# Kernel tuning notes

Hardware: AMD Instinct MI355X
Metric: run time of the kernel (lower is better)

The kernel has to match this reference:

```python
import jax, jax.numpy as jnp
import numpy as np
from jax import lax

B, C, H, W = 4, 64, 128, 128
G, K, CO = 8, 3, 64
KK = K * K
MC = G * KK  # mask channels = 72


def _conv3x3(x, w, b):
    # standard 3x3 conv, stride 1, padding 1, NCHW
    y = lax.conv_general_dilated(x, w, (1, 1), ((1, 1), (1, 1)),
                                 dimension_numbers=('NCHW', 'OIHW', 'NCHW'))
    return y + b[None, :, None, None]


def _deform_conv2d(x, offset, mask, w, b):
    """Modulated deformable conv (DCNv2), stride=1, padding=1, dilation=1.
    offset: [B, 2*G*KK, H, W] interpreted as [B, G, KK, 2(dy,dx), H, W] (torchvision layout).
    mask:   [B, G*KK, H, W].
    w: [Co, C/G, K, K], b: [Co].
    """
    Bn, Cn, Hn, Wn = x.shape
    Co, Cg, Kh, Kw = w.shape
    Gn = Cn // Cg
    KKn = Kh * Kw
    Ho, Wo = Hn, Wn  # stride 1, pad 1, k 3

    off = offset.reshape(Bn, Gn, KKn, 2, Ho, Wo)
    dy, dx = off[:, :, :, 0], off[:, :, :, 1]
    m = mask.reshape(Bn, Gn, 1, KKn, Ho, Wo)

    kh = (jnp.arange(KKn) // Kw).astype(x.dtype)  # kernel row index
    kw = (jnp.arange(KKn) % Kw).astype(x.dtype)
    hh = jnp.arange(Ho, dtype=x.dtype)
    ww = jnp.arange(Wo, dtype=x.dtype)
    # sampling positions: h - pad + kh*dil + dy  -> [B,G,KK,Ho,Wo]
    py = hh[None, None, None, :, None] - 1.0 + kh[None, None, :, None, None] + dy
    px = ww[None, None, None, None, :] - 1.0 + kw[None, None, :, None, None] + dx

    y0 = jnp.floor(py); x0 = jnp.floor(px)
    ly = py - y0; lx = px - x0
    y0i = y0.astype(jnp.int32); x0i = x0.astype(jnp.int32)
    y1i = y0i + 1; x1i = x0i + 1

    xg = x.reshape(Bn, Gn, Cg, Hn * Wn)

    def corner(yi, xi, wgt):
        valid = ((yi >= 0) & (yi < Hn) & (xi >= 0) & (xi < Wn)).astype(x.dtype)
        idx = (jnp.clip(yi, 0, Hn - 1) * Wn + jnp.clip(xi, 0, Wn - 1))
        idx = idx.reshape(Bn, Gn, 1, KKn * Ho * Wo)
        v = jnp.take_along_axis(xg, idx, axis=3).reshape(Bn, Gn, Cg, KKn, Ho, Wo)
        return v * (wgt * valid)[:, :, None]

    val = (corner(y0i, x0i, (1.0 - ly) * (1.0 - lx))
           + corner(y0i, x1i, (1.0 - ly) * lx)
           + corner(y1i, x0i, ly * (1.0 - lx))
           + corner(y1i, x1i, ly * lx))
    val = val * m  # modulation

    wr = w.reshape(Gn, Co // Gn, Cg, KKn)
    out = jnp.einsum('bgckhw,gock->bgohw', val, wr).reshape(Bn, Co, Ho, Wo)
    return out + b[None, :, None, None]


def setup_inputs() -> dict:
    key = jax.random.key(0)
    ks = jax.random.split(key, 8)
    f = lambda k, s, sc=1.0: jax.random.normal(k, s, dtype=jnp.float32) * sc
    return {
        'x': f(ks[0], (B, C, H, W)),
        'share_with_feat': f(ks[1], (B, C, H, W)),
        'offset_feat': f(ks[2], (B, C, H, W)),
        # conv_offset_mask: C -> 3*G*KK (zero-init in original; small random here)
        'w_om': f(ks[3], (3 * MC, C, 3, 3), 0.02),
        'b_om': jnp.zeros((3 * MC,), jnp.float32),
        'w_em1': f(ks[4], (C, 2 * C, 3, 3), 0.05),
        'b_em1': jnp.zeros((C,), jnp.float32),
        'w_em2': f(ks[5], (MC, C, 3, 3), 0.05),
        'b_em2': jnp.zeros((MC,), jnp.float32),
        # deform conv weight: [Co, C/G, 3, 3]
        'w_dc': f(ks[6], (CO, C // G, 3, 3), 0.05),
        'b_dc': f(ks[7], (CO,), 0.05),
    }


def reference(x, share_with_feat, offset_feat, w_om, b_om, w_em1, b_em1,
              w_em2, b_em2, w_dc, b_dc):
    om = _conv3x3(offset_feat, w_om, b_om)
    o1, o2, mask_x = jnp.split(om, 3, axis=1)
    offset = jnp.concatenate([o1, o2], axis=1)
    mask_x = jax.nn.sigmoid(mask_x)
    x_deform = _deform_conv2d(x, offset, mask_x, w_dc, b_dc)
    # extra_mask=True branch
    em = _conv3x3(jnp.concatenate([share_with_feat, offset_feat], axis=1), w_em1, b_em1)
    em = jnp.where(em >= 0, em, 0.1 * em)  # LeakyReLU(0.1)
    em = jax.nn.sigmoid(_conv3x3(em, w_em2, b_em2))
    share_deform = _deform_conv2d(share_with_feat, offset, em, w_dc, b_dc)
    return (x_deform, share_deform)
```

## Files before the change

### kernel.cpp

```cpp
#include <hip/hip_runtime.h>
#include <math.h>

#define BB 4
#define CC 64
#define HH 128
#define WW 128
#define GG 8
#define COO 64
#define HWC (HH*WW)

#define DPAD 12
#define DROW 26

typedef float f32x16 __attribute__((ext_vector_type(16)));
typedef __bf16 bf16x8 __attribute__((ext_vector_type(8)));

__device__ __forceinline__ unsigned short bf16_rn(float f) {
    unsigned int u = __float_as_uint(f);
    unsigned int r = (u + 0x7fffu + ((u >> 16) & 1u)) >> 16;
    return (unsigned short)r;
}
__device__ __forceinline__ float b2f(unsigned short u) {
    return __uint_as_float(((unsigned int)u) << 16);
}

__global__ __launch_bounds__(256) void to_c16_kernel(const float* __restrict__ in,
                                                     unsigned short* __restrict__ out) {
    __shared__ unsigned short lds[64][66];
    const int b = blockIdx.y;
    const int pix0 = blockIdx.x * 64;
    const int t = threadIdx.x;
    {
        const int p = t & 63, q = t >> 6;
#pragma unroll
        for (int i = 0; i < 16; i++) {
            int c = i * 4 + q;
            lds[c][p] = bf16_rn(in[((size_t)b * 64 + c) * HWC + pix0 + p]);
        }
    }
    __syncthreads();
    {
        const int pl = t & 63, cg = t >> 6;
        unsigned int u[8];
#pragma unroll
        for (int j = 0; j < 8; j++) {
            unsigned int lo = lds[cg * 16 + 2 * j][pl];
            unsigned int hi = lds[cg * 16 + 2 * j + 1][pl];
            u[j] = lo | (hi << 16);
        }
        unsigned int* dst = (unsigned int*)(out + ((size_t)(b * 4 + cg) * HWC + pix0 + pl) * 16);
        *(uint4*)dst = make_uint4(u[0], u[1], u[2], u[3]);
        *(uint4*)(dst + 4) = make_uint4(u[4], u[5], u[6], u[7]);
    }
}

__global__ __launch_bounds__(256) void pack_xs_kernel(const float* __restrict__ x,
                                                      const float* __restrict__ s,
                                                      unsigned int* __restrict__ xs, int n) {
    int i = blockIdx.x * 256 + threadIdx.x;
    if (i < n) {
        xs[i] = (unsigned int)bf16_rn(x[i]) | ((unsigned int)bf16_rn(s[i]) << 16);
    }
}

__global__ void pack_w_kernel(const float* __restrict__ w, unsigned short* __restrict__ wp,
                              int Cout, int COP, int CinTot, int n) {
    int idx = blockIdx.x * 256 + threadIdx.x;
    if (idx >= n) return;
    int i  = idx & 15;
    int co = (idx >> 4) % COP;
    int t  = idx / (16 * COP);
    int cg = t & 3;
    int kk = (t >> 2) % 9;
    int seg = t / 36;
    int cin = seg * 64 + cg * 16 + i;
    float v = (co < Cout) ? w[((size_t)co * CinTot + cin) * 9 + kk] : 0.f;
    wp[idx] = bf16_rn(v);
}

template<int NSEG>
__global__ __launch_bounds__(256) void conv_mfma_kernel(
    const unsigned short* __restrict__ in0,
    const unsigned short* __restrict__ in1,
    const unsigned short* __restrict__ wp,
    const float* __restrict__ bias,
    void* __restrict__ out,
    int Cout, int COP, int out_mode, int act)
{
    const int lane = threadIdx.x & 63;
    const int wid  = threadIdx.x >> 6;
    const int l31  = lane & 31;
    const int half = lane >> 5;
    const int b    = blockIdx.x >> 5;
    const int r    = ((blockIdx.x & 31) << 2) + wid;
    const int co0  = blockIdx.y * 32;

    f32x16 acc[4];
#pragma unroll
    for (int nt = 0; nt < 4; nt++)
#pragma unroll
        for (int rg = 0; rg < 16; rg++) acc[nt][rg] = 0.f;

    bf16x8 bz;
#pragma unroll
    for (int i = 0; i < 8; i++) bz[i] = (__bf16)0.f;

#pragma unroll
    for (int seg = 0; seg < NSEG; seg++) {
        const unsigned short* in = seg ? in1 : in0;
        const unsigned short* inb = in + (size_t)b * 4 * HWC * 16;
        for (int kk = 0; kk < 9; kk++) {
            const int rr = r + kk / 3 - 1;
            if ((unsigned)rr < (unsigned)HH) {
                const int dxo = kk % 3 - 1;
#pragma unroll
                for (int cg = 0; cg < 4; cg++) {
                    bf16x8 afrag = *(const bf16x8*)(wp +
                        ((size_t)(((seg * 9 + kk) * 4 + cg) * COP + co0 + l31) * 16 + half * 8));
                    const size_t plane = ((size_t)cg * HWC + (size_t)rr * WW) * 16;
#pragma unroll
                    for (int nt = 0; nt < 4; nt++) {
                        const int cc = nt * 32 + l31 + dxo;
                        bf16x8 bfrag = bz;
                        if ((unsigned)cc < (unsigned)WW)
                            bfrag = *(const bf16x8*)(inb + plane + (size_t)cc * 16 + half * 8);
                        acc[nt] = __builtin_amdgcn_mfma_f32_32x32x16_bf16(afrag, bfrag, acc[nt], 0, 0, 0);
                    }
                }
            }
        }
    }

#pragma unroll
    for (int nt = 0; nt < 4; nt++) {
#pragma unroll
        for (int rg = 0; rg < 16; rg++) {
            const int row = (rg & 3) + 8 * (rg >> 2) + 4 * half;
            const int co = co0 + row;
            if (co < Cout) {
                float v = acc[nt][rg] + bias[co];
                if (act == 1)      v = (v >= 0.f) ? v : 0.1f * v;
                else if (act == 2) v = 1.f / (1.f + __expf(-v));
                else if (act == 3 && co >= 144) v = 1.f / (1.f + __expf(-v));
                const int pix = r * WW + nt * 32 + l31;
                if (out_mode == 2)
                    ((unsigned short*)out)[((size_t)b * Cout + co) * HWC + pix] = bf16_rn(v);
                else
                    ((unsigned short*)out)[((size_t)(b * 4 + (co >> 4)) * HWC + pix) * 16 + (co & 15)] = bf16_rn(v);
            }
        }
    }
}

__global__ __launch_bounds__(256) void deform_fused_kernel(
    const unsigned int* __restrict__ xs,
    const unsigned short* __restrict__ om, const unsigned short* __restrict__ em,
    const float* __restrict__ wdc, const float* __restrict__ bdc,
    float* __restrict__ outx, float* __restrict__ outs)
{
    __shared__ __align__(16) unsigned int lds[24 * DROW * DPAD];

    const int bg = blockIdx.x >> 6;
    const int b = bg >> 3, g = bg & 7;
    const int tile = blockIdx.x & 63;
    const int r0 = (tile >> 3) << 4;
    const int c0 = (tile & 7) << 4;
    const int tx = threadIdx.x & 15, ty = threadIdx.x >> 4;
    const int h = r0 + ty, w = c0 + tx;
    const int wr0 = r0 - 4, wc0 = c0 - 4;

    const unsigned int* xsb = xs + ((size_t)b * 64 + g * 8) * HWC;

#pragma unroll
    for (int i = 0; i < 18; i++) {
        unsigned int slot = (unsigned int)threadIdx.x + i * 256u;
        unsigned int sx = slot % 24u;
        unsigned int t2 = slot / 24u;
        unsigned int sy = t2 % 24u;
        unsigned int c  = t2 / 24u;
        int iy = min(max(wr0 + (int)sy, 0), HH - 1);
        int ix = min(max(wc0 + (int)sx, 0), WW - 1);
        lds[(sy * DROW + sx) * DPAD + c] = xsb[(size_t)c * HWC + iy * WW + ix];
    }

    __syncthreads();

    const int pix = h * WW + w;
    const unsigned short* omb = om + (size_t)b * 216 * HWC + pix + (size_t)g * 18 * HWC;
    const unsigned short* mmb = om + (size_t)b * 216 * HWC + pix + (size_t)(144 + g * 9) * HWC;
    const unsigned short* emb = em + (size_t)b * 72 * HWC + pix + (size_t)g * 9 * HWC;

    float accx[8], accs[8];
#pragma unroll
    for (int o = 0; o < 8; o++) { accx[o] = 0.f; accs[o] = 0.f; }

#pragma unroll
    for (int kk = 0; kk < 9; kk++) {
        const float dy = b2f(omb[(size_t)(kk * 2) * HWC]);
        const float dx = b2f(omb[(size_t)(kk * 2 + 1) * HWC]);
        const float m1 = b2f(mmb[(size_t)kk * HWC]);
        const float m2 = b2f(emb[(size_t)kk * HWC]);

        const float py = (float)(h - 1 + kk / 3) + dy;
        const float px = (float)(w - 1 + kk % 3) + dx;
        const float y0f = floorf(py), x0f = floorf(px);
        const float ly = py - y0f, lx = px - x0f;
        const int y0 = (int)y0f, x0 = (int)x0f;
        const int y1 = y0 + 1, x1 = x0 + 1;
        const bool vy0 = (y0 >= 0) && (y0 < HH), vy1 = (y1 >= 0) && (y1 < HH);
        const bool vx0 = (x0 >= 0) && (x0 < WW), vx1 = (x1 >= 0) && (x1 < WW);
        float w00 = (1.f - ly) * (1.f - lx); if (!(vy0 && vx0)) w00 = 0.f;
        float w01 = (1.f - ly) * lx;         if (!(vy0 && vx1)) w01 = 0.f;
        float w10 = ly * (1.f - lx);         if (!(vy1 && vx0)) w10 = 0.f;
        float w11 = ly * lx;                 if (!(vy1 && vx1)) w11 = 0.f;
        const int cy0 = min(max(y0, 0), HH - 1), cy1 = min(max(y1, 0), HH - 1);
        const int cx0 = min(max(x0, 0), WW - 1), cx1 = min(max(x1, 0), WW - 1);

        const int sy0 = cy0 - wr0, sy1 = cy1 - wr0;
        const int sx0 = cx0 - wc0, sx1 = cx1 - wc0;
        const bool inw = (sy0 >= 0) && (sy1 < 24) && (sx0 >= 0) && (sx1 < 24);

        const float* wk = wdc + (size_t)g * 8 * 8 * 9 + kk;

        if (__builtin_expect(inw, 1)) {
            const int p00 = (sy0 * DROW + sx0) * DPAD, p01 = (sy0 * DROW + sx1) * DPAD;
            const int p10 = (sy1 * DROW + sx0) * DPAD, p11 = (sy1 * DROW + sx1) * DPAD;
#pragma unroll
            for (int ch = 0; ch < 2; ch++) {
                uint4 qa = *(const uint4*)(lds + p00 + ch * 4);
                uint4 qb = *(const uint4*)(lds + p01 + ch * 4);
                uint4 qc = *(const uint4*)(lds + p10 + ch * 4);
                uint4 qd = *(const uint4*)(lds + p11 + ch * 4);
                const unsigned int ua[4] = {qa.x, qa.y, qa.z, qa.w};
                const unsigned int ub[4] = {qb.x, qb.y, qb.z, qb.w};
                const unsigned int uc[4] = {qc.x, qc.y, qc.z, qc.w};
                const unsigned int ud[4] = {qd.x, qd.y, qd.z, qd.w};
#pragma unroll
                for (int j = 0; j < 4; j++) {
                    const int c = ch * 4 + j;
                    float x00 = __uint_as_float(ua[j] << 16), s00 = __uint_as_float(ua[j] & 0xffff0000u);
                    float x01 = __uint_as_float(ub[j] << 16), s01 = __uint_as_float(ub[j] & 0xffff0000u);
                    float x10 = __uint_as_float(uc[j] << 16), s10 = __uint_as_float(uc[j] & 0xffff0000u);
                    float x11 = __uint_as_float(ud[j] << 16), s11 = __uint_as_float(ud[j] & 0xffff0000u);
                    float vx = w00 * x00; vx = fmaf(w01, x01, vx); vx = fmaf(w10, x10, vx); vx = fmaf(w11, x11, vx);
                    float vs = w00 * s00; vs = fmaf(w01, s01, vs); vs = fmaf(w10, s10, vs); vs = fmaf(w11, s11, vs);
                    vx *= m1;
                    vs *= m2;
#pragma unroll
                    for (int o = 0; o < 8; o++) {
                        const float wv = wk[(size_t)(o * 8 + c) * 9];
                        accx[o] = fmaf(vx, wv, accx[o]);
                        accs[o] = fmaf(vs, wv, accs[o]);
                    }
                }
            }
        } else {
            const int i00 = cy0 * WW + cx0, i01 = cy0 * WW + cx1;
            const int i10 = cy1 * WW + cx0, i11 = cy1 * WW + cx1;
#pragma unroll
            for (int c = 0; c < 8; c++) {
                const unsigned int* xc = xsb + (size_t)c * HWC;
                unsigned int a = xc[i00], bq = xc[i01], cq = xc[i10], dq = xc[i11];
                float x00 = __uint_as_float(a << 16),  s00 = __uint_as_float(a & 0xffff0000u);
                float x01 = __uint_as_float(bq << 16), s01 = __uint_as_float(bq & 0xffff0000u);
                float x10 = __uint_as_float(cq << 16), s10 = __uint_as_float(cq & 0xffff0000u);
                float x11 = __uint_as_float(dq << 16), s11 = __uint_as_float(dq & 0xffff0000u);
                float vx = w00 * x00; vx = fmaf(w01, x01, vx); vx = fmaf(w10, x10, vx); vx = fmaf(w11, x11, vx);
                float vs = w00 * s00; vs = fmaf(w01, s01, vs); vs = fmaf(w10, s10, vs); vs = fmaf(w11, s11, vs);
                vx *= m1;
                vs *= m2;
#pragma unroll
                for (int o = 0; o < 8; o++) {
                    const float wv = wk[(size_t)(o * 8 + c) * 9];
                    accx[o] = fmaf(vx, wv, accx[o]);
                    accs[o] = fmaf(vs, wv, accs[o]);
                }
            }
        }
    }

#pragma unroll
    for (int o = 0; o < 8; o++) {
        const float bv = bdc[g * 8 + o];
        outx[((size_t)(b * COO + g * 8 + o)) * HWC + pix] = accx[o] + bv;
        outs[((size_t)(b * COO + g * 8 + o)) * HWC + pix] = accs[o] + bv;
    }
}

extern "C" void kernel_launch(void* const* d_in, const int* in_sizes, int n_in,
                              void* d_out, int out_size, void* d_ws, size_t ws_size,
                              hipStream_t stream) {
    const float* x      = (const float*)d_in[0];
    const float* share  = (const float*)d_in[1];
    const float* offf   = (const float*)d_in[2];
    const float* w_om   = (const float*)d_in[3];
    const float* b_om   = (const float*)d_in[4];
    const float* w_em1  = (const float*)d_in[5];
    const float* b_em1  = (const float*)d_in[6];
    const float* w_em2  = (const float*)d_in[7];
    const float* b_em2  = (const float*)d_in[8];
    const float* w_dc   = (const float*)d_in[9];
    const float* b_dc   = (const float*)d_in[10];

    unsigned int* xs = (unsigned int*)d_ws;
    unsigned short* us = (unsigned short*)(xs + 4194304);
    unsigned short* sc16   = us;
    unsigned short* oc16   = sc16 + 4194304;
    unsigned short* emm    = oc16 + 4194304;
    unsigned short* om_b   = emm + 4194304;
    unsigned short* em_b   = om_b + 14155776;
    unsigned short* wp_om  = em_b + 4718592;
    unsigned short* wp_em1 = wp_om + 129024;
    unsigned short* wp_em2 = wp_em1 + 73728;

    float* outx = (float*)d_out;
    float* outs = outx + 4194304;

    dim3 blk(256);

    pack_xs_kernel<<<(4194304 + 255) / 256, blk, 0, stream>>>(x, share, xs, 4194304);
    to_c16_kernel<<<dim3(HWC / 64, BB), blk, 0, stream>>>(share, sc16);
    to_c16_kernel<<<dim3(HWC / 64, BB), blk, 0, stream>>>(offf, oc16);

    pack_w_kernel<<<(129024 + 255) / 256, blk, 0, stream>>>(w_om,  wp_om,  216, 224, 64,  129024);
    pack_w_kernel<<<(73728  + 255) / 256, blk, 0, stream>>>(w_em1, wp_em1, 64,  64,  128, 73728);
    pack_w_kernel<<<(55296  + 255) / 256, blk, 0, stream>>>(w_em2, wp_em2, 72,  96,  64,  55296);

    conv_mfma_kernel<1><<<dim3(BB * HH / 4, 7), blk, 0, stream>>>(
        oc16, nullptr, wp_om, b_om, om_b, 216, 224, 2, 3);
    conv_mfma_kernel<2><<<dim3(BB * HH / 4, 2), blk, 0, stream>>>(
        sc16, oc16, wp_em1, b_em1, emm, 64, 64, 3, 1);
    conv_mfma_kernel<1><<<dim3(BB * HH / 4, 3), blk, 0, stream>>>(
        emm, nullptr, wp_em2, b_em2, em_b, 72, 96, 2, 2);

    deform_fused_kernel<<<dim3(BB * GG * 64), blk, 0, stream>>>(
        xs, om_b, em_b, w_dc, b_dc, outx, outs);
}
```

Measured before the change: 331.4 us.

## Fuse input/weight packing kernels and split conv tiles along width for occupancy

Merges the three input-conversion kernels into one pass that reads share once, and merges the three weight-pack launches into a single kernel, cutting launch count and a redundant read of share. The MFMA conv kernel gains an NT template parameter so each block covers part of a row; this multiplies the grid size and lowers per-wave accumulator registers, raising occupancy on the small convs. It also unrolls the kernel-tap loop and replaces the row-bounds branch with a clamped row plus a zeroed A fragment. The cost is reloading the weight fragments once per width slice and some extra loads for out-of-range rows.

```diff
diff --git a/kernel.cpp b/kernel.cpp
--- a/kernel.cpp
+++ b/kernel.cpp
@@ -24,23 +24,29 @@
     return __uint_as_float(((unsigned int)u) << 16);
 }
 
-__global__ __launch_bounds__(256) void to_c16_kernel(const float* __restrict__ in,
-                                                     unsigned short* __restrict__ out) {
+__global__ __launch_bounds__(256) void pack_inputs_kernel(
+    const float* __restrict__ x, const float* __restrict__ share,
+    const float* __restrict__ offf,
+    unsigned int* __restrict__ xs, unsigned short* __restrict__ sc16,
+    unsigned short* __restrict__ oc16)
+{
     __shared__ unsigned short lds[64][66];
     const int b = blockIdx.y;
     const int pix0 = blockIdx.x * 64;
     const int t = threadIdx.x;
-    {
-        const int p = t & 63, q = t >> 6;
-#pragma unroll
-        for (int i = 0; i < 16; i++) {
-            int c = i * 4 + q;
-            lds[c][p] = bf16_rn(in[((size_t)b * 64 + c) * HWC + pix0 + p]);
-        }
+    const int p = t & 63, q = t >> 6;
+    const int pl = t & 63, cg = t >> 6;
+
+#pragma unroll
+    for (int i = 0; i < 16; i++) {
+        int c = i * 4 + q;
+        size_t idx = ((size_t)b * 64 + c) * HWC + pix0 + p;
+        unsigned short sb = bf16_rn(share[idx]);
+        lds[c][p] = sb;
+        xs[idx] = (unsigned int)bf16_rn(x[idx]) | ((unsigned int)sb << 16);
     }
     __syncthreads();
     {
-        const int pl = t & 63, cg = t >> 6;
         unsigned int u[8];
 #pragma unroll
         for (int j = 0; j < 8; j++) {
@@ -48,25 +54,35 @@
             unsigned int hi = lds[cg * 16 + 2 * j + 1][pl];
             u[j] = lo | (hi << 16);
         }
-        unsigned int* dst = (unsigned int*)(out + ((size_t)(b * 4 + cg) * HWC + pix0 + pl) * 16);
+        unsigned int* dst = (unsigned int*)(sc16 + ((size_t)(b * 4 + cg) * HWC + pix0 + pl) * 16);
         *(uint4*)dst = make_uint4(u[0], u[1], u[2], u[3]);
         *(uint4*)(dst + 4) = make_uint4(u[4], u[5], u[6], u[7]);
     }
-}
-
-__global__ __launch_bounds__(256) void pack_xs_kernel(const float* __restrict__ x,
-                                                      const float* __restrict__ s,
-                                                      unsigned int* __restrict__ xs, int n) {
-    int i = blockIdx.x * 256 + threadIdx.x;
-    if (i < n) {
-        xs[i] = (unsigned int)bf16_rn(x[i]) | ((unsigned int)bf16_rn(s[i]) << 16);
-    }
-}
-
-__global__ void pack_w_kernel(const float* __restrict__ w, unsigned short* __restrict__ wp,
-                              int Cout, int COP, int CinTot, int n) {
-    int idx = blockIdx.x * 256 + threadIdx.x;
-    if (idx >= n) return;
+    __syncthreads();
+
+#pragma unroll
+    for (int i = 0; i < 16; i++) {
+        int c = i * 4 + q;
+        lds[c][p] = bf16_rn(offf[((size_t)b * 64 + c) * HWC + pix0 + p]);
+    }
+    __syncthreads();
+    {
+        unsigned int u[8];
+#pragma unroll
+        for (int j = 0; j < 8; j++) {
+            unsigned int lo = lds[cg * 16 + 2 * j][pl];
+            unsigned int hi = lds[cg * 16 + 2 * j + 1][pl];
+            u[j] = lo | (hi << 16);
+        }
+        unsigned int* dst = (unsigned int*)(oc16 + ((size_t)(b * 4 + cg) * HWC + pix0 + pl) * 16);
+        *(uint4*)dst = make_uint4(u[0], u[1], u[2], u[3]);
+        *(uint4*)(dst + 4) = make_uint4(u[4], u[5], u[6], u[7]);
+    }
+}
+
+__device__ __forceinline__ void pack_w_one(const float* __restrict__ w,
+                                           unsigned short* __restrict__ wp,
+                                           int Cout, int COP, int CinTot, int idx) {
     int i  = idx & 15;
     int co = (idx >> 4) % COP;
     int t  = idx / (16 * COP);
@@ -78,7 +94,20 @@
     wp[idx] = bf16_rn(v);
 }
 
-template<int NSEG>
+__global__ void pack_w_all_kernel(const float* __restrict__ w_om, unsigned short* __restrict__ wp_om,
+                                  const float* __restrict__ w_em1, unsigned short* __restrict__ wp_em1,
+                                  const float* __restrict__ w_em2, unsigned short* __restrict__ wp_em2) {
+    int i = blockIdx.x * 256 + threadIdx.x;
+    if (i < 129024) {
+        pack_w_one(w_om, wp_om, 216, 224, 64, i);
+    } else if (i < 129024 + 73728) {
+        pack_w_one(w_em1, wp_em1, 64, 64, 128, i - 129024);
+    } else if (i < 129024 + 73728 + 55296) {
+        pack_w_one(w_em2, wp_em2, 72, 96, 64, i - 129024 - 73728);
+    }
+}
+
+template<int NSEG, int NT>
 __global__ __launch_bounds__(256) void conv_mfma_kernel(
     const unsigned short* __restrict__ in0,
     const unsigned short* __restrict__ in1,
@@ -87,17 +116,22 @@
     void* __restrict__ out,
     int Cout, int COP, int out_mode, int act)
 {
+    constexpr int XS = 128 / (NT * 32);
     const int lane = threadIdx.x & 63;
     const int wid  = threadIdx.x >> 6;
     const int l31  = lane & 31;
     const int half = lane >> 5;
-    const int b    = blockIdx.x >> 5;
-    const int r    = ((blockIdx.x & 31) << 2) + wid;
-    const int co0  = blockIdx.y * 32;
-
-    f32x16 acc[4];
-#pragma unroll
-    for (int nt = 0; nt < 4; nt++)
+    int tmp = blockIdx.x;
+    const int xsp = tmp % XS; tmp /= XS;
+    const int rb  = tmp % (HH / 4);
+    const int b   = tmp / (HH / 4);
+    const int r   = rb * 4 + wid;
+    const int px0 = xsp * NT * 32;
+    const int co0 = blockIdx.y * 32;
+
+    f32x16 acc[NT];
+#pragma unroll
+    for (int nt = 0; nt < NT; nt++)
 #pragma unroll
         for (int rg = 0; rg < 16; rg++) acc[nt][rg] = 0.f;
 
@@ -109,30 +143,32 @@
     for (int seg = 0; seg < NSEG; seg++) {
         const unsigned short* in = seg ? in1 : in0;
         const unsigned short* inb = in + (size_t)b * 4 * HWC * 16;
+#pragma unroll
         for (int kk = 0; kk < 9; kk++) {
             const int rr = r + kk / 3 - 1;
-            if ((unsigned)rr < (unsigned)HH) {
-                const int dxo = kk % 3 - 1;
-#pragma unroll
-                for (int cg = 0; cg < 4; cg++) {
-                    bf16x8 afrag = *(const bf16x8*)(wp +
-                        ((size_t)(((seg * 9 + kk) * 4 + cg) * COP + co0 + l31) * 16 + half * 8));
-                    const size_t plane = ((size_t)cg * HWC + (size_t)rr * WW) * 16;
-#pragma unroll
-                    for (int nt = 0; nt < 4; nt++) {
-                        const int cc = nt * 32 + l31 + dxo;
-                        bf16x8 bfrag = bz;
-                        if ((unsigned)cc < (unsigned)WW)
-                            bfrag = *(const bf16x8*)(inb + plane + (size_t)cc * 16 + half * 8);
-                        acc[nt] = __builtin_amdgcn_mfma_f32_32x32x16_bf16(afrag, bfrag, acc[nt], 0, 0, 0);
-                    }
+            const bool rv = (unsigned)rr < (unsigned)HH;
+            const int rrc = min(max(rr, 0), HH - 1);
+            const int dxo = kk % 3 - 1;
+#pragma unroll
+            for (int cg = 0; cg < 4; cg++) {
+                bf16x8 afrag = *(const bf16x8*)(wp +
+                    ((size_t)(((seg * 9 + kk) * 4 + cg) * COP + co0 + l31) * 16 + half * 8));
+                if (!rv) afrag = bz;
+                const size_t plane = ((size_t)cg * HWC + (size_t)rrc * WW) * 16;
+#pragma unroll
+                for (int nt = 0; nt < NT; nt++) {
+                    const int cc = px0 + nt * 32 + l31 + dxo;
+                    bf16x8 bfrag = bz;
+                    if ((unsigned)cc < (unsigned)WW)
+                        bfrag = *(const bf16x8*)(inb + plane + (size_t)cc * 16 + half * 8);
+                    acc[nt] = __builtin_amdgcn_mfma_f32_32x32x16_bf16(afrag, bfrag, acc[nt], 0, 0, 0);
                 }
             }
         }
     }
 
 #pragma unroll
-    for (int nt = 0; nt < 4; nt++) {
+    for (int nt = 0; nt < NT; nt++) {
 #pragma unroll
         for (int rg = 0; rg < 16; rg++) {
             const int row = (rg & 3) + 8 * (rg >> 2) + 4 * half;
@@ -142,7 +178,7 @@
                 if (act == 1)      v = (v >= 0.f) ? v : 0.1f * v;
                 else if (act == 2) v = 1.f / (1.f + __expf(-v));
                 else if (act == 3 && co >= 144) v = 1.f / (1.f + __expf(-v));
-                const int pix = r * WW + nt * 32 + l31;
+                const int pix = r * WW + px0 + nt * 32 + l31;
                 if (out_mode == 2)
                     ((unsigned short*)out)[((size_t)b * Cout + co) * HWC + pix] = bf16_rn(v);
                 else
@@ -318,19 +354,15 @@
 
     dim3 blk(256);
 
-    pack_xs_kernel<<<(4194304 + 255) / 256, blk, 0, stream>>>(x, share, xs, 4194304);
-    to_c16_kernel<<<dim3(HWC / 64, BB), blk, 0, stream>>>(share, sc16);
-    to_c16_kernel<<<dim3(HWC / 64, BB), blk, 0, stream>>>(offf, oc16);
-
-    pack_w_kernel<<<(129024 + 255) / 256, blk, 0, stream>>>(w_om,  wp_om,  216, 224, 64,  129024);
-    pack_w_kernel<<<(73728  + 255) / 256, blk, 0, stream>>>(w_em1, wp_em1, 64,  64,  128, 73728);
-    pack_w_kernel<<<(55296  + 255) / 256, blk, 0, stream>>>(w_em2, wp_em2, 72,  96,  64,  55296);
-
-    conv_mfma_kernel<1><<<dim3(BB * HH / 4, 7), blk, 0, stream>>>(
+    pack_inputs_kernel<<<dim3(HWC / 64, BB), blk, 0, stream>>>(x, share, offf, xs, sc16, oc16);
+    pack_w_all_kernel<<<(258048 + 255) / 256, blk, 0, stream>>>(
+        w_om, wp_om, w_em1, wp_em1, w_em2, wp_em2);
+
+    conv_mfma_kernel<1, 2><<<dim3(BB * (HH / 4) * 2, 7), blk, 0, stream>>>(
         oc16, nullptr, wp_om, b_om, om_b, 216, 224, 2, 3);
-    conv_mfma_kernel<2><<<dim3(BB * HH / 4, 2), blk, 0, stream>>>(
+    conv_mfma_kernel<2, 1><<<dim3(BB * (HH / 4) * 4, 2), blk, 0, stream>>>(
         sc16, oc16, wp_em1, b_em1, emm, 64, 64, 3, 1);
-    conv_mfma_kernel<1><<<dim3(BB * HH / 4, 3), blk, 0, stream>>>(
+    conv_mfma_kernel<1, 1><<<dim3(BB * (HH / 4) * 4, 3), blk, 0, stream>>>(
         emm, nullptr, wp_em2, b_em2, em_b, 72, 96, 2, 2);
 
     deform_fused_kernel<<<dim3(BB * GG * 64), blk, 0, stream>>>(
```

New measurement: 276.1 us. 16.7% less time.
